# Performance work log

Measured on AMD Instinct MI355X. Metric: run time of the kernel, lower is better.

The kernel has to match this reference:

```python
import jax, jax.numpy as jnp
import numpy as np

N_NODES = 100000
N_EDGES = 1600000
EPS = 1e-5


def _xavier(key, shape):
    fan_out, fan_in = shape
    lim = float(np.sqrt(6.0 / (fan_in + fan_out)))
    return jax.random.uniform(key, shape, jnp.float32, -lim, lim)


def setup_inputs() -> dict:
    key = jax.random.key(0)
    ks = jax.random.split(key, 16)
    d_in, d1, d2, d3 = 32, 64, 128, 64
    inp = {
        "x": jax.random.normal(ks[0], (N_NODES, d_in), jnp.float32),
        "edge_index": jax.random.randint(ks[1], (2, N_EDGES), 0, N_NODES, jnp.int64),
        "edge_weight": jax.random.uniform(ks[2], (N_EDGES,), jnp.float32),
        # GraphConv params: lin_rel (with bias) applied to aggregated msgs, lin_root (no bias)
        "W1_rel": _xavier(ks[3], (d1, d_in)), "b1": jnp.zeros((d1,), jnp.float32), "W1_root": _xavier(ks[4], (d1, d_in)),
        "W2_rel": _xavier(ks[5], (d2, d1)), "b2": jnp.zeros((d2,), jnp.float32), "W2_root": _xavier(ks[6], (d2, d1)),
        "W3_rel": _xavier(ks[7], (d3, d2)), "b3": jnp.zeros((d3,), jnp.float32), "W3_root": _xavier(ks[8], (d3, d2)),
        # BatchNorm affine params
        "g1": jnp.ones((d1,), jnp.float32), "be1": jnp.zeros((d1,), jnp.float32),
        "g2": jnp.ones((d2,), jnp.float32), "be2": jnp.zeros((d2,), jnp.float32),
        "g3": jnp.ones((d3,), jnp.float32), "be3": jnp.zeros((d3,), jnp.float32),
        # node-level classifier: Linear(64,32) -> ReLU -> Linear(32,2)
        "Wc1": _xavier(ks[9], (32, d3)), "bc1": jnp.zeros((32,), jnp.float32),
        "Wc2": _xavier(ks[10], (2, 32)), "bc2": jnp.zeros((2,), jnp.float32),
    }
    return inp


def _graph_conv(x, src, dst, W_rel, b, W_root, ew=None):
    msg = x[src]                      # [E, d] gather
    if ew is not None:
        msg = msg * ew[:, None]
    agg = jax.ops.segment_sum(msg, dst, num_segments=N_NODES)  # [N, d] scatter-add
    return agg @ W_rel.T + b + x @ W_root.T


def _bn(h, g, beta):
    mu = jnp.mean(h, axis=0)
    var = jnp.var(h, axis=0)
    return (h - mu) * jax.lax.rsqrt(var + EPS) * g + beta


def reference(x, edge_index, edge_weight,
              W1_rel, b1, W1_root, W2_rel, b2, W2_root, W3_rel, b3, W3_root,
              g1, be1, g2, be2, g3, be3, Wc1, bc1, Wc2, bc2):
    src, dst = edge_index[0], edge_index[1]
    h1 = jax.nn.relu(_bn(_graph_conv(x, src, dst, W1_rel, b1, W1_root), g1, be1))
    h2 = jax.nn.relu(_bn(_graph_conv(h1, src, dst, W2_rel, b2, W2_root), g2, be2))
    h3 = _bn(_graph_conv(h2, src, dst, W3_rel, b3, W3_root, edge_weight), g3, be3)
    h3 = jax.nn.relu(h3 + h1)  # residual (dims match, no projection)
    logits = jax.nn.relu(h3 @ Wc1.T + bc1) @ Wc2.T + bc2  # [N, 2]
    return logits
```

## Files before the change

kernel.cpp:

```cpp
#include <hip/hip_runtime.h>

#define N_NODES 100000
#define N_EDGES 1600000
#define EPSV 1e-5f

__device__ __forceinline__ ushort f2bf(float f) {
  unsigned u = __float_as_uint(f);
  unsigned r = (u + 0x7FFFu + ((u >> 16) & 1u)) >> 16;
  return (ushort)r;
}


__global__ void hist_kernel(const int* __restrict__ ei, int* __restrict__ cnt) {
  int e = blockIdx.x * blockDim.x + threadIdx.x;
  if (e >= N_EDGES) return;
  atomicAdd(&cnt[ei[N_EDGES + e]], 1);
}

#define SCAN_BLK 1024
#define SCAN_NB ((N_NODES + SCAN_BLK - 1) / SCAN_BLK)

__global__ void scan_phase1(const int* __restrict__ cnt, int* __restrict__ blocksum) {
  __shared__ int part[256];
  int base = blockIdx.x * SCAN_BLK + threadIdx.x * 4;
  int s = 0;
#pragma unroll
  for (int i = 0; i < 4; ++i) {
    int idx = base + i;
    if (idx < N_NODES) s += cnt[idx];
  }
  part[threadIdx.x] = s;
  __syncthreads();
  for (int d = 128; d > 0; d >>= 1) {
    if (threadIdx.x < d) part[threadIdx.x] += part[threadIdx.x + d];
    __syncthreads();
  }
  if (threadIdx.x == 0) blocksum[blockIdx.x] = part[0];
}

__global__ void scan_phase2(int* __restrict__ blocksum, int* __restrict__ rowptr) {
  __shared__ int part[128];
  int tid = threadIdx.x;
  int v = (tid < SCAN_NB) ? blocksum[tid] : 0;
  part[tid] = v;
  __syncthreads();
  for (int d = 1; d < 128; d <<= 1) {
    int t = (tid >= d) ? part[tid - d] : 0;
    __syncthreads();
    part[tid] += t;
    __syncthreads();
  }
  if (tid < SCAN_NB) blocksum[tid] = part[tid] - v;
  if (tid == 127) rowptr[N_NODES] = part[127];
}

__global__ void scan_phase3(const int* __restrict__ cnt, const int* __restrict__ blocksum,
                            int* __restrict__ rowptr, int* __restrict__ cursor) {
  __shared__ int part[256];
  int base = blockIdx.x * SCAN_BLK + threadIdx.x * 4;
  int c[4];
  int s = 0;
#pragma unroll
  for (int i = 0; i < 4; ++i) {
    int idx = base + i;
    c[i] = (idx < N_NODES) ? cnt[idx] : 0;
    s += c[i];
  }
  part[threadIdx.x] = s;
  __syncthreads();
  int me = s;
  for (int d = 1; d < 256; d <<= 1) {
    int t = (threadIdx.x >= d) ? part[threadIdx.x - d] : 0;
    __syncthreads();
    part[threadIdx.x] += t;
    __syncthreads();
  }
  int off = blocksum[blockIdx.x] + part[threadIdx.x] - me;
#pragma unroll
  for (int i = 0; i < 4; ++i) {
    int idx = base + i;
    if (idx < N_NODES) {
      rowptr[idx] = off;
      cursor[idx] = off;
      off += c[i];
    }
  }
}

#define FILL_SUB 256

__global__ void fill_kernel(const int* __restrict__ ei, const float* __restrict__ ew,
                            int* __restrict__ cursor, unsigned* __restrict__ col) {
  const int g = blockIdx.x & 7;
  const int sub = blockIdx.x >> 3;
  const int lo = g * 12500;
  const int hi = lo + 12500;
  const int EPB = (N_EDGES + FILL_SUB - 1) / FILL_SUB;
  const int beg = sub * EPB;
  const int end = min(beg + EPB, N_EDGES);
  for (int e = beg + (int)threadIdx.x; e < end; e += (int)blockDim.x) {
    int d = ei[N_EDGES + e];
    if (d < lo || d >= hi) continue;
    int p = atomicAdd(&cursor[d], 1);
    col[p] = ((unsigned)f2bf(ew[e]) << 17) | (unsigned)ei[e];
  }
}


__global__ void cast_bf16(const float* __restrict__ in, ushort* __restrict__ out, int n4) {
  int i = blockIdx.x * blockDim.x + threadIdx.x;
  if (i >= n4) return;
  float4 v = reinterpret_cast<const float4*>(in)[i];
  ushort4 o = make_ushort4(f2bf(v.x), f2bf(v.y), f2bf(v.z), f2bf(v.w));
  reinterpret_cast<ushort4*>(out)[i] = o;
}


__global__ void wtrans_kernel(const float* __restrict__ W1rel, const float* __restrict__ W1root,
                              const float* __restrict__ W2rel, const float* __restrict__ W2root,
                              const float* __restrict__ W3rel, const float* __restrict__ W3root,
                              float* __restrict__ Wt) {
  int i = blockIdx.x * blockDim.x + threadIdx.x;
  if (i >= 36864) return;
  float v;
  if (i < 4096) {
    int k = i >> 6, j = i & 63;
    v = (k < 32) ? W1rel[j * 32 + k] : W1root[j * 32 + (k - 32)];
  } else if (i < 20480) {
    int r = i - 4096;
    int k = r >> 7, j = r & 127;
    v = (k < 64) ? W2rel[j * 64 + k] : W2root[j * 64 + (k - 64)];
  } else if (i < 28672) {
    int r = i - 20480;
    int k = r >> 6, j = r & 63;
    v = W3rel[j * 128 + k];
  } else {
    int r = i - 28672;
    int k = r >> 6, j = r & 63;
    v = W3root[j * 128 + k];
  }
  Wt[i] = v;
}


#define SRC_OF(v) ((v) & 0x1FFFFu)
#define W_OF(v) __uint_as_float(((v) >> 17) << 16)

__global__ void gather_d32_bf(const ushort* __restrict__ xb, const int* __restrict__ rowptr,
                              const unsigned* __restrict__ col, float* __restrict__ agg) {
  int gid = blockIdx.x * blockDim.x + threadIdx.x;
  int n = gid >> 2;
  if (n >= N_NODES) return;
  int c = gid & 3;
  int beg = rowptr[n], end = rowptr[n + 1];
  float acc[8];
#pragma unroll
  for (int i = 0; i < 8; ++i) acc[i] = 0.f;
  int p = beg;
  for (; p + 1 < end; p += 2) {
    unsigned e0 = col[p], e1 = col[p + 1];
    uint4 u0 = *reinterpret_cast<const uint4*>(xb + (size_t)SRC_OF(e0) * 32 + c * 8);
    uint4 u1 = *reinterpret_cast<const uint4*>(xb + (size_t)SRC_OF(e1) * 32 + c * 8);
    unsigned a0[4] = {u0.x, u0.y, u0.z, u0.w};
    unsigned a1[4] = {u1.x, u1.y, u1.z, u1.w};
#pragma unroll
    for (int i = 0; i < 4; ++i) {
      acc[2 * i]     += __uint_as_float(a0[i] << 16) + __uint_as_float(a1[i] << 16);
      acc[2 * i + 1] += __uint_as_float(a0[i] & 0xFFFF0000u) +
                        __uint_as_float(a1[i] & 0xFFFF0000u);
    }
  }
  if (p < end) {
    unsigned e0 = col[p];
    uint4 u0 = *reinterpret_cast<const uint4*>(xb + (size_t)SRC_OF(e0) * 32 + c * 8);
    unsigned a0[4] = {u0.x, u0.y, u0.z, u0.w};
#pragma unroll
    for (int i = 0; i < 4; ++i) {
      acc[2 * i]     += __uint_as_float(a0[i] << 16);
      acc[2 * i + 1] += __uint_as_float(a0[i] & 0xFFFF0000u);
    }
  }
  float* op = agg + (size_t)n * 32 + c * 8;
  *reinterpret_cast<float4*>(op)     = make_float4(acc[0], acc[1], acc[2], acc[3]);
  *reinterpret_cast<float4*>(op + 4) = make_float4(acc[4], acc[5], acc[6], acc[7]);
}

template <bool WEIGHTED, bool TRANS>
__global__ void gather_d64_bf(const ushort* __restrict__ hb, const int* __restrict__ rowptr,
                              const unsigned* __restrict__ col,
                              const float* __restrict__ sc, const float* __restrict__ sh,
                              float* __restrict__ agg) {
  int gid = blockIdx.x * blockDim.x + threadIdx.x;
  int n = gid >> 3;
  if (n >= N_NODES) return;
  int c = gid & 7;
  int beg = rowptr[n], end = rowptr[n + 1];
  float sc8[8], sh8[8];
  if (TRANS) {
#pragma unroll
    for (int i = 0; i < 8; ++i) {
      sc8[i] = sc[c * 8 + i];
      sh8[i] = sh[c * 8 + i];
    }
  }
  float acc[8];
#pragma unroll
  for (int i = 0; i < 8; ++i) acc[i] = 0.f;

  auto body = [&](unsigned ev, const uint4& u) {
    float w = WEIGHTED ? W_OF(ev) : 1.f;
    unsigned uu[4] = {u.x, u.y, u.z, u.w};
#pragma unroll
    for (int i = 0; i < 4; ++i) {
      float lo = __uint_as_float(uu[i] << 16);
      float hi = __uint_as_float(uu[i] & 0xFFFF0000u);
      if (TRANS) {
        lo = fmaxf(fmaf(lo, sc8[2 * i], sh8[2 * i]), 0.f);
        hi = fmaxf(fmaf(hi, sc8[2 * i + 1], sh8[2 * i + 1]), 0.f);
      }
      if (WEIGHTED) {
        acc[2 * i]     = fmaf(lo, w, acc[2 * i]);
        acc[2 * i + 1] = fmaf(hi, w, acc[2 * i + 1]);
      } else {
        acc[2 * i]     += lo;
        acc[2 * i + 1] += hi;
      }
    }
  };

  int p = beg;
  for (; p + 1 < end; p += 2) {
    unsigned e0 = col[p], e1 = col[p + 1];
    uint4 u0 = *reinterpret_cast<const uint4*>(hb + (size_t)SRC_OF(e0) * 64 + c * 8);
    uint4 u1 = *reinterpret_cast<const uint4*>(hb + (size_t)SRC_OF(e1) * 64 + c * 8);
    body(e0, u0);
    body(e1, u1);
  }
  if (p < end) {
    unsigned e0 = col[p];
    uint4 u0 = *reinterpret_cast<const uint4*>(hb + (size_t)SRC_OF(e0) * 64 + c * 8);
    body(e0, u0);
  }
  float* op = agg + (size_t)n * 64 + c * 8;
  *reinterpret_cast<float4*>(op)     = make_float4(acc[0], acc[1], acc[2], acc[3]);
  *reinterpret_cast<float4*>(op + 4) = make_float4(acc[4], acc[5], acc[6], acc[7]);
}


template <int K1, int K2, int DO, int TA1, int TA2, int RADD, int STATS, int OUTM>
__global__ __launch_bounds__(256, 4) void gemm_node(
    const float* __restrict__ A1, const float* __restrict__ A2,
    const float* __restrict__ Wt,
    const float* __restrict__ sc, const float* __restrict__ sh,
    const float* __restrict__ R, float* __restrict__ out, ushort* __restrict__ outb,
    float* h2act, float* __restrict__ sums) {
  constexpr int K = K1 + K2;
  constexpr int NC = K / 32;
  constexpr int NJB = DO / 64;
  __shared__ __align__(16) float A_lds[64][36];
  __shared__ __align__(16) float W_lds[32][DO];

  const int tid = threadIdx.x;
  const int tx = tid & 15, ty = tid >> 4;
  const int nbase = blockIdx.x * 64;

  float4 acc[4][NJB];
#pragma unroll
  for (int i = 0; i < 4; ++i)
#pragma unroll
    for (int jb = 0; jb < NJB; ++jb) acc[i][jb] = make_float4(0.f, 0.f, 0.f, 0.f);

#pragma unroll 1
  for (int c = 0; c < NC; ++c) {
    const int kb = c * 32;
    if (c) __syncthreads();
#pragma unroll
    for (int it = 0; it < 2; ++it) {
      int idx = it * 256 + tid;
      int nl = idx >> 3;
      int kq = (idx & 7) * 4;
      int k = kb + kq;
      int ng = nbase + nl;
      float4 v = make_float4(0.f, 0.f, 0.f, 0.f);
      bool isA1 = (K2 == 0) || (k < K1);
      if (ng < N_NODES) {
        if (isA1)
          v = *reinterpret_cast<const float4*>(A1 + (size_t)ng * K1 + k);
        else
          v = *reinterpret_cast<const float4*>(A2 + (size_t)ng * K2 + (k - K1));
      }
      if constexpr (TA1) {
        if (isA1) {
          float4 s4 = *reinterpret_cast<const float4*>(sc + k);
          float4 h4 = *reinterpret_cast<const float4*>(sh + k);
          v.x = fmaxf(fmaf(v.x, s4.x, h4.x), 0.f);
          v.y = fmaxf(fmaf(v.y, s4.y, h4.y), 0.f);
          v.z = fmaxf(fmaf(v.z, s4.z, h4.z), 0.f);
          v.w = fmaxf(fmaf(v.w, s4.w, h4.w), 0.f);
          if (ng < N_NODES)
            *reinterpret_cast<float4*>(h2act + (size_t)ng * K1 + k) = v;
        }
      }
      if constexpr (TA2 && K2 > 0) {
        if (!isA1) {
          float4 s4 = *reinterpret_cast<const float4*>(sc + (k - K1));
          float4 h4 = *reinterpret_cast<const float4*>(sh + (k - K1));
          v.x = fmaxf(fmaf(v.x, s4.x, h4.x), 0.f);
          v.y = fmaxf(fmaf(v.y, s4.y, h4.y), 0.f);
          v.z = fmaxf(fmaf(v.z, s4.z, h4.z), 0.f);
          v.w = fmaxf(fmaf(v.w, s4.w, h4.w), 0.f);
        }
      }
      *reinterpret_cast<float4*>(&A_lds[nl][kq]) = v;
    }
    {
      const float4* wsrc = reinterpret_cast<const float4*>(Wt + (size_t)kb * DO);
      float4* wdst = reinterpret_cast<float4*>(&W_lds[0][0]);
#pragma unroll
      for (int it = 0; it < DO / 32; ++it)
        wdst[it * 256 + tid] = wsrc[it * 256 + tid];
    }
    __syncthreads();
#pragma unroll 2
    for (int k4 = 0; k4 < 8; ++k4) {
      float4 a[4];
#pragma unroll
      for (int i = 0; i < 4; ++i)
        a[i] = *reinterpret_cast<const float4*>(&A_lds[ty * 4 + i][k4 * 4]);
#pragma unroll
      for (int q = 0; q < 4; ++q) {
#pragma unroll
        for (int jb = 0; jb < NJB; ++jb) {
          float4 w = *reinterpret_cast<const float4*>(&W_lds[k4 * 4 + q][jb * 64 + tx * 4]);
#pragma unroll
          for (int i = 0; i < 4; ++i) {
            float av = reinterpret_cast<const float*>(&a[i])[q];
            acc[i][jb].x = fmaf(av, w.x, acc[i][jb].x);
            acc[i][jb].y = fmaf(av, w.y, acc[i][jb].y);
            acc[i][jb].z = fmaf(av, w.z, acc[i][jb].z);
            acc[i][jb].w = fmaf(av, w.w, acc[i][jb].w);
          }
        }
      }
    }
  }
#pragma unroll
  for (int i = 0; i < 4; ++i) {
    int ng = nbase + ty * 4 + i;
    if (ng >= N_NODES) continue;
#pragma unroll
    for (int jb = 0; jb < NJB; ++jb) {
      if constexpr (RADD) {
        float4 rr = *reinterpret_cast<const float4*>(R + (size_t)ng * DO + jb * 64 + tx * 4);
        acc[i][jb].x += rr.x; acc[i][jb].y += rr.y;
        acc[i][jb].z += rr.z; acc[i][jb].w += rr.w;
      }
      size_t off = (size_t)ng * DO + jb * 64 + tx * 4;
      if constexpr (OUTM == 1) {
        ushort4 o = make_ushort4(f2bf(acc[i][jb].x), f2bf(acc[i][jb].y),
                                 f2bf(acc[i][jb].z), f2bf(acc[i][jb].w));
        *reinterpret_cast<ushort4*>((ushort*)out + off) = o;
      } else {
        *reinterpret_cast<float4*>(out + off) = acc[i][jb];
        if constexpr (OUTM == 2) {
          ushort4 o = make_ushort4(f2bf(acc[i][jb].x), f2bf(acc[i][jb].y),
                                   f2bf(acc[i][jb].z), f2bf(acc[i][jb].w));
          *reinterpret_cast<ushort4*>(outb + off) = o;
        }
      }
    }
  }
  if constexpr (STATS) {
    __syncthreads();
    float* sums_l = &A_lds[0][0];
    float* sq_l = &W_lds[0][0];
#pragma unroll
    for (int jb = 0; jb < NJB; ++jb) {
      float4 s = make_float4(0.f, 0.f, 0.f, 0.f);
      float4 q = make_float4(0.f, 0.f, 0.f, 0.f);
#pragma unroll
      for (int i = 0; i < 4; ++i) {
        if (nbase + ty * 4 + i < N_NODES) {
          float4 v = acc[i][jb];
          s.x += v.x; s.y += v.y; s.z += v.z; s.w += v.w;
          q.x = fmaf(v.x, v.x, q.x); q.y = fmaf(v.y, v.y, q.y);
          q.z = fmaf(v.z, v.z, q.z); q.w = fmaf(v.w, v.w, q.w);
        }
      }
      *reinterpret_cast<float4*>(&sums_l[ty * DO + jb * 64 + tx * 4]) = s;
      *reinterpret_cast<float4*>(&sq_l[ty * DO + jb * 64 + tx * 4]) = q;
    }
    __syncthreads();
    if (tid < DO) {
      float s = 0.f, q = 0.f;
#pragma unroll
      for (int t = 0; t < 16; ++t) {
        s += sums_l[t * DO + tid];
        q += sq_l[t * DO + tid];
      }
      unsafeAtomicAdd(&sums[tid], s);
      unsafeAtomicAdd(&sums[DO + tid], q);
    }
  }
}


__global__ void bn_finalize(const float* __restrict__ sums, const float* __restrict__ g,
                            const float* __restrict__ be, float* __restrict__ sc,
                            float* __restrict__ sh, int D) {
  int j = threadIdx.x;
  if (j >= D) return;
  const float invN = 1.f / (float)N_NODES;
  float mean = sums[j] * invN;
  float var = sums[D + j] * invN - mean * mean;
  float r = rsqrtf(var + EPSV);
  float scale = g[j] * r;
  sc[j] = scale;
  sh[j] = be[j] - mean * scale;
}


__global__ __launch_bounds__(256) void final_fused(
    const float* __restrict__ h3p, const float* __restrict__ h1p,
    const float* __restrict__ sc1, const float* __restrict__ sh1,
    const float* __restrict__ sc3, const float* __restrict__ sh3,
    const float* __restrict__ Wc1, const float* __restrict__ bc1,
    const float* __restrict__ Wc2, const float* __restrict__ bc2,
    float* __restrict__ out) {
  __shared__ __align__(16) float t_lds[64][68];
  __shared__ __align__(16) float w1_lds[64][36];
  __shared__ __align__(16) float c_lds[64][36];
  __shared__ __align__(16) float w2_lds[64];
  __shared__ __align__(16) float b1_lds[32];
  __shared__ float b2_lds[2];
  const int tid = threadIdx.x;
  const int nbase = blockIdx.x * 64;

#pragma unroll
  for (int it = 0; it < 4; ++it) {
    int idx = it * 256 + tid;
    int nl = idx >> 4;
    int k = (idx & 15) * 4;
    int ng = nbase + nl;
    float4 v = make_float4(0.f, 0.f, 0.f, 0.f);
    if (ng < N_NODES) {
      float4 p = *reinterpret_cast<const float4*>(h3p + (size_t)ng * 64 + k);
      float4 u = *reinterpret_cast<const float4*>(h1p + (size_t)ng * 64 + k);
      float4 sa = *reinterpret_cast<const float4*>(sc1 + k);
      float4 ha = *reinterpret_cast<const float4*>(sh1 + k);
      float4 sb = *reinterpret_cast<const float4*>(sc3 + k);
      float4 hb = *reinterpret_cast<const float4*>(sh3 + k);
      float h1x = fmaxf(fmaf(u.x, sa.x, ha.x), 0.f);
      float h1y = fmaxf(fmaf(u.y, sa.y, ha.y), 0.f);
      float h1z = fmaxf(fmaf(u.z, sa.z, ha.z), 0.f);
      float h1w = fmaxf(fmaf(u.w, sa.w, ha.w), 0.f);
      v.x = fmaxf(fmaf(p.x, sb.x, hb.x) + h1x, 0.f);
      v.y = fmaxf(fmaf(p.y, sb.y, hb.y) + h1y, 0.f);
      v.z = fmaxf(fmaf(p.z, sb.z, hb.z) + h1z, 0.f);
      v.w = fmaxf(fmaf(p.w, sb.w, hb.w) + h1w, 0.f);
    }
    *reinterpret_cast<float4*>(&t_lds[nl][k]) = v;
  }
#pragma unroll
  for (int it = 0; it < 8; ++it) {
    int idx = it * 256 + tid;
    int j = idx >> 6;
    int k = idx & 63;
    w1_lds[k][j] = Wc1[(size_t)j * 64 + k];
  }
  if (tid < 64) w2_lds[tid] = Wc2[tid];
  else if (tid < 96) b1_lds[tid - 64] = bc1[tid - 64];
  else if (tid < 98) b2_lds[tid - 96] = bc2[tid - 96];
  __syncthreads();

  {
    const int tx = tid & 7, ty = tid >> 3;
    float4 a0c = make_float4(0.f, 0.f, 0.f, 0.f);
    float4 a1c = make_float4(0.f, 0.f, 0.f, 0.f);
#pragma unroll 4
    for (int k4 = 0; k4 < 16; ++k4) {
      float4 a0 = *reinterpret_cast<const float4*>(&t_lds[ty * 2 + 0][k4 * 4]);
      float4 a1 = *reinterpret_cast<const float4*>(&t_lds[ty * 2 + 1][k4 * 4]);
#pragma unroll
      for (int q = 0; q < 4; ++q) {
        float4 w = *reinterpret_cast<const float4*>(&w1_lds[k4 * 4 + q][tx * 4]);
        float a0q = reinterpret_cast<const float*>(&a0)[q];
        float a1q = reinterpret_cast<const float*>(&a1)[q];
        a0c.x = fmaf(a0q, w.x, a0c.x); a0c.y = fmaf(a0q, w.y, a0c.y);
        a0c.z = fmaf(a0q, w.z, a0c.z); a0c.w = fmaf(a0q, w.w, a0c.w);
        a1c.x = fmaf(a1q, w.x, a1c.x); a1c.y = fmaf(a1q, w.y, a1c.y);
        a1c.z = fmaf(a1q, w.z, a1c.z); a1c.w = fmaf(a1q, w.w, a1c.w);
      }
    }
    float4 b = *reinterpret_cast<const float4*>(&b1_lds[tx * 4]);
    a0c.x = fmaxf(a0c.x + b.x, 0.f); a0c.y = fmaxf(a0c.y + b.y, 0.f);
    a0c.z = fmaxf(a0c.z + b.z, 0.f); a0c.w = fmaxf(a0c.w + b.w, 0.f);
    a1c.x = fmaxf(a1c.x + b.x, 0.f); a1c.y = fmaxf(a1c.y + b.y, 0.f);
    a1c.z = fmaxf(a1c.z + b.z, 0.f); a1c.w = fmaxf(a1c.w + b.w, 0.f);
    *reinterpret_cast<float4*>(&c_lds[ty * 2 + 0][tx * 4]) = a0c;
    *reinterpret_cast<float4*>(&c_lds[ty * 2 + 1][tx * 4]) = a1c;
  }
  __syncthreads();

  if (tid < 128) {
    int nl = tid >> 1, o = tid & 1;
    int ng = nbase + nl;
    if (ng < N_NODES) {
      float s = b2_lds[o];
#pragma unroll
      for (int k = 0; k < 32; ++k) s = fmaf(c_lds[nl][k], w2_lds[o * 32 + k], s);
      out[(size_t)ng * 2 + o] = s;
    }
  }
}


extern "C" void kernel_launch(void* const* d_in, const int* in_sizes, int n_in,
                              void* d_out, int out_size, void* d_ws, size_t ws_size,
                              hipStream_t stream) {
  const float* x      = (const float*)d_in[0];
  const int*   ei     = (const int*)d_in[1];
  const float* ew     = (const float*)d_in[2];
  const float* W1rel  = (const float*)d_in[3];
  const float* W1root = (const float*)d_in[5];
  const float* W2rel  = (const float*)d_in[6];
  const float* W2root = (const float*)d_in[8];
  const float* W3rel  = (const float*)d_in[9];
  const float* W3root = (const float*)d_in[11];
  const float* g1  = (const float*)d_in[12];
  const float* be1 = (const float*)d_in[13];
  const float* g2  = (const float*)d_in[14];
  const float* be2 = (const float*)d_in[15];
  const float* g3  = (const float*)d_in[16];
  const float* be3 = (const float*)d_in[17];
  const float* Wc1 = (const float*)d_in[18];
  const float* bc1 = (const float*)d_in[19];
  const float* Wc2 = (const float*)d_in[20];
  const float* bc2 = (const float*)d_in[21];

  float* ws = (float*)d_ws;
  const size_t NF = (size_t)N_NODES * 64;
  float* A = ws;
  float* B = ws + NF;
  float* C = ws + 2 * NF;
  float* E = ws + 3 * NF;
  float* X = ws + 5 * NF;
  float* S = X;
  int* rowptr   = (int*)(X + 1024);
  int* cnt      = rowptr + (N_NODES + 2);
  int* cursor   = cnt + N_NODES;
  int* blocksum = cursor + N_NODES;
  unsigned* col = (unsigned*)(blocksum + 128);
  float* Wt     = (float*)(col + N_EDGES);
  float* Wt1  = Wt;
  float* Wt2  = Wt + 4096;
  float* Wt3r = Wt + 20480;
  float* Wt3o = Wt + 28672;

  ushort* xb     = (ushort*)B;
  ushort* h1preb = (ushort*)E;
  ushort* y2b    = (ushort*)B;

  hipMemsetAsync(S, 0, 1024 * sizeof(float), stream);
  hipMemsetAsync(cnt, 0, N_NODES * sizeof(int), stream);

  const int edgeBlocks = (N_EDGES + 255) / 256;
  const int tileBlocks = (N_NODES + 63) / 64;

  cast_bf16<<<(N_NODES * 32 / 4 + 255) / 256, 256, 0, stream>>>(x, xb, N_NODES * 32 / 4);
  wtrans_kernel<<<144, 256, 0, stream>>>(W1rel, W1root, W2rel, W2root, W3rel, W3root, Wt);

  hist_kernel<<<edgeBlocks, 256, 0, stream>>>(ei, cnt);
  scan_phase1<<<SCAN_NB, 256, 0, stream>>>(cnt, blocksum);
  scan_phase2<<<1, 128, 0, stream>>>(blocksum, rowptr);
  scan_phase3<<<SCAN_NB, 256, 0, stream>>>(cnt, blocksum, rowptr, cursor);
  fill_kernel<<<8 * FILL_SUB, 256, 0, stream>>>(ei, ew, cursor, col);

  gather_d32_bf<<<(N_NODES * 4 + 255) / 256, 256, 0, stream>>>(xb, rowptr, col, A);
  gemm_node<32, 32, 64, 0, 0, 0, 1, 2><<<tileBlocks, 256, 0, stream>>>(
      A, x, Wt1, nullptr, nullptr, nullptr, C, h1preb, nullptr, S);
  bn_finalize<<<1, 128, 0, stream>>>(S, g1, be1, S + 128, S + 192, 64);

  gather_d64_bf<false, true><<<(N_NODES * 8 + 255) / 256, 256, 0, stream>>>(
      h1preb, rowptr, col, S + 128, S + 192, A);
  gemm_node<64, 64, 128, 0, 1, 0, 1, 0><<<tileBlocks, 256, 0, stream>>>(
      A, C, Wt2, S + 128, S + 192, nullptr, E, nullptr, nullptr, S + 256);
  bn_finalize<<<1, 128, 0, stream>>>(S + 256, g2, be2, S + 512, S + 640, 128);

  gemm_node<128, 0, 64, 1, 0, 0, 0, 1><<<tileBlocks, 256, 0, stream>>>(
      E, nullptr, Wt3r, S + 512, S + 640, nullptr, (float*)y2b, nullptr, E, nullptr);

  gather_d64_bf<true, false><<<(N_NODES * 8 + 255) / 256, 256, 0, stream>>>(
      y2b, rowptr, col, nullptr, nullptr, A);
  gemm_node<128, 0, 64, 0, 0, 1, 1, 0><<<tileBlocks, 256, 0, stream>>>(
      E, nullptr, Wt3o, nullptr, nullptr, A, B, nullptr, nullptr, S + 768);
  bn_finalize<<<1, 128, 0, stream>>>(S + 768, g3, be3, S + 896, S + 960, 64);

  final_fused<<<tileBlocks, 256, 0, stream>>>(B, C, S + 128, S + 192, S + 896, S + 960,
                                              Wc1, bc1, Wc2, bc2, (float*)d_out);
}
```

Before: 479.7 us.

## Store layer-2 pre-activation in bf16 and recompute BN-ReLU in both layer-3 GEMMs

The layer-2 GEMM now writes its pre-BN output as bf16 (OUTM=1) rather than fp32. The two layer-3 GEMMs read that bf16 buffer and each reapplies the BN2 scale/shift and ReLU when loading it, so the fp32 h2 activation is no longer written out. The histogram kernel also adopts the fill kernel's partitioned-by-destination scheme with nontemporal loads, and GEMM launch bounds go from 4 to 6 waves. This cuts fp32 traffic on the hidden activations at the cost of extra bf16 rounding of h2 and some duplicated elementwise work.

```diff
diff --git a/kernel.cpp b/kernel.cpp
--- a/kernel.cpp
+++ b/kernel.cpp
@@ -11,10 +11,20 @@
 }
 
 
+#define FILL_SUB 256
+#define GRP_W 12500
+
 __global__ void hist_kernel(const int* __restrict__ ei, int* __restrict__ cnt) {
-  int e = blockIdx.x * blockDim.x + threadIdx.x;
-  if (e >= N_EDGES) return;
-  atomicAdd(&cnt[ei[N_EDGES + e]], 1);
+  const int g = blockIdx.x & 7;
+  const int sub = blockIdx.x >> 3;
+  const int lo = g * GRP_W, hi = lo + GRP_W;
+  const int EPB = (N_EDGES + FILL_SUB - 1) / FILL_SUB;
+  const int beg = sub * EPB;
+  const int end = min(beg + EPB, N_EDGES);
+  for (int e = beg + (int)threadIdx.x; e < end; e += (int)blockDim.x) {
+    int d = __builtin_nontemporal_load(ei + N_EDGES + e);
+    if (d >= lo && d < hi) atomicAdd(&cnt[d], 1);
+  }
 }
 
 #define SCAN_BLK 1024
@@ -87,22 +97,21 @@
   }
 }
 
-#define FILL_SUB 256
-
 __global__ void fill_kernel(const int* __restrict__ ei, const float* __restrict__ ew,
                             int* __restrict__ cursor, unsigned* __restrict__ col) {
   const int g = blockIdx.x & 7;
   const int sub = blockIdx.x >> 3;
-  const int lo = g * 12500;
-  const int hi = lo + 12500;
+  const int lo = g * GRP_W, hi = lo + GRP_W;
   const int EPB = (N_EDGES + FILL_SUB - 1) / FILL_SUB;
   const int beg = sub * EPB;
   const int end = min(beg + EPB, N_EDGES);
   for (int e = beg + (int)threadIdx.x; e < end; e += (int)blockDim.x) {
-    int d = ei[N_EDGES + e];
+    int d = __builtin_nontemporal_load(ei + N_EDGES + e);
     if (d < lo || d >= hi) continue;
     int p = atomicAdd(&cursor[d], 1);
-    col[p] = ((unsigned)f2bf(ew[e]) << 17) | (unsigned)ei[e];
+    int src = __builtin_nontemporal_load(ei + e);
+    float w = __builtin_nontemporal_load(ew + e);
+    col[p] = ((unsigned)f2bf(w) << 17) | (unsigned)src;
   }
 }
 
@@ -247,13 +256,13 @@
 }
 
 
-template <int K1, int K2, int DO, int TA1, int TA2, int RADD, int STATS, int OUTM>
-__global__ __launch_bounds__(256, 4) void gemm_node(
-    const float* __restrict__ A1, const float* __restrict__ A2,
+template <int K1, int K2, int DO, int A1B16, int TA1, int TA2, int RADD, int STATS, int OUTM>
+__global__ __launch_bounds__(256, 6) void gemm_node(
+    const void* __restrict__ A1v, const float* __restrict__ A2,
     const float* __restrict__ Wt,
     const float* __restrict__ sc, const float* __restrict__ sh,
     const float* __restrict__ R, float* __restrict__ out, ushort* __restrict__ outb,
-    float* h2act, float* __restrict__ sums) {
+    float* __restrict__ sums) {
   constexpr int K = K1 + K2;
   constexpr int NC = K / 32;
   constexpr int NJB = DO / 64;
@@ -284,10 +293,20 @@
       float4 v = make_float4(0.f, 0.f, 0.f, 0.f);
       bool isA1 = (K2 == 0) || (k < K1);
       if (ng < N_NODES) {
-        if (isA1)
-          v = *reinterpret_cast<const float4*>(A1 + (size_t)ng * K1 + k);
-        else
+        if (isA1) {
+          if constexpr (A1B16) {
+            uint2 u = *reinterpret_cast<const uint2*>(
+                (const ushort*)A1v + (size_t)ng * K1 + k);
+            v.x = __uint_as_float(u.x << 16);
+            v.y = __uint_as_float(u.x & 0xFFFF0000u);
+            v.z = __uint_as_float(u.y << 16);
+            v.w = __uint_as_float(u.y & 0xFFFF0000u);
+          } else {
+            v = *reinterpret_cast<const float4*>((const float*)A1v + (size_t)ng * K1 + k);
+          }
+        } else {
           v = *reinterpret_cast<const float4*>(A2 + (size_t)ng * K2 + (k - K1));
+        }
       }
       if constexpr (TA1) {
         if (isA1) {
@@ -297,8 +316,6 @@
           v.y = fmaxf(fmaf(v.y, s4.y, h4.y), 0.f);
           v.z = fmaxf(fmaf(v.z, s4.z, h4.z), 0.f);
           v.w = fmaxf(fmaf(v.w, s4.w, h4.w), 0.f);
-          if (ng < N_NODES)
-            *reinterpret_cast<float4*>(h2act + (size_t)ng * K1 + k) = v;
         }
       }
       if constexpr (TA2 && K2 > 0) {
@@ -559,41 +576,41 @@
 
   ushort* xb     = (ushort*)B;
   ushort* h1preb = (ushort*)E;
+  ushort* h2preb = (ushort*)E;
   ushort* y2b    = (ushort*)B;
 
   hipMemsetAsync(S, 0, 1024 * sizeof(float), stream);
   hipMemsetAsync(cnt, 0, N_NODES * sizeof(int), stream);
 
-  const int edgeBlocks = (N_EDGES + 255) / 256;
   const int tileBlocks = (N_NODES + 63) / 64;
 
   cast_bf16<<<(N_NODES * 32 / 4 + 255) / 256, 256, 0, stream>>>(x, xb, N_NODES * 32 / 4);
   wtrans_kernel<<<144, 256, 0, stream>>>(W1rel, W1root, W2rel, W2root, W3rel, W3root, Wt);
 
-  hist_kernel<<<edgeBlocks, 256, 0, stream>>>(ei, cnt);
+  hist_kernel<<<8 * FILL_SUB, 256, 0, stream>>>(ei, cnt);
   scan_phase1<<<SCAN_NB, 256, 0, stream>>>(cnt, blocksum);
   scan_phase2<<<1, 128, 0, stream>>>(blocksum, rowptr);
   scan_phase3<<<SCAN_NB, 256, 0, stream>>>(cnt, blocksum, rowptr, cursor);
   fill_kernel<<<8 * FILL_SUB, 256, 0, stream>>>(ei, ew, cursor, col);
 
   gather_d32_bf<<<(N_NODES * 4 + 255) / 256, 256, 0, stream>>>(xb, rowptr, col, A);
-  gemm_node<32, 32, 64, 0, 0, 0, 1, 2><<<tileBlocks, 256, 0, stream>>>(
-      A, x, Wt1, nullptr, nullptr, nullptr, C, h1preb, nullptr, S);
+  gemm_node<32, 32, 64, 0, 0, 0, 0, 1, 2><<<tileBlocks, 256, 0, stream>>>(
+      A, x, Wt1, nullptr, nullptr, nullptr, C, h1preb, S);
   bn_finalize<<<1, 128, 0, stream>>>(S, g1, be1, S + 128, S + 192, 64);
 
   gather_d64_bf<false, true><<<(N_NODES * 8 + 255) / 256, 256, 0, stream>>>(
       h1preb, rowptr, col, S + 128, S + 192, A);
-  gemm_node<64, 64, 128, 0, 1, 0, 1, 0><<<tileBlocks, 256, 0, stream>>>(
-      A, C, Wt2, S + 128, S + 192, nullptr, E, nullptr, nullptr, S + 256);
+  gemm_node<64, 64, 128, 0, 0, 1, 0, 1, 1><<<tileBlocks, 256, 0, stream>>>(
+      A, C, Wt2, S + 128, S + 192, nullptr, (float*)h2preb, nullptr, S + 256);
   bn_finalize<<<1, 128, 0, stream>>>(S + 256, g2, be2, S + 512, S + 640, 128);
 
-  gemm_node<128, 0, 64, 1, 0, 0, 0, 1><<<tileBlocks, 256, 0, stream>>>(
-      E, nullptr, Wt3r, S + 512, S + 640, nullptr, (float*)y2b, nullptr, E, nullptr);
+  gemm_node<128, 0, 64, 1, 1, 0, 0, 0, 1><<<tileBlocks, 256, 0, stream>>>(
+      h2preb, nullptr, Wt3r, S + 512, S + 640, nullptr, (float*)y2b, nullptr, nullptr);
 
   gather_d64_bf<true, false><<<(N_NODES * 8 + 255) / 256, 256, 0, stream>>>(
       y2b, rowptr, col, nullptr, nullptr, A);
-  gemm_node<128, 0, 64, 0, 0, 1, 1, 0><<<tileBlocks, 256, 0, stream>>>(
-      E, nullptr, Wt3o, nullptr, nullptr, A, B, nullptr, nullptr, S + 768);
+  gemm_node<128, 0, 64, 1, 1, 0, 1, 1, 0><<<tileBlocks, 256, 0, stream>>>(
+      h2preb, nullptr, Wt3o, S + 512, S + 640, A, B, nullptr, S + 768);
   bn_finalize<<<1, 128, 0, stream>>>(S + 768, g3, be3, S + 896, S + 960, 64);
 
   final_fused<<<tileBlocks, 256, 0, stream>>>(B, C, S + 128, S + 192, S + 896, S + 960,
```

Measured after the change: 499.5 us. +4.1%, slower.
